# Optimization experiments

Measured on AMD Instinct MI355X. Metric: run time of the kernel, lower is better.

## Reference

```python
import jax, jax.numpy as jnp
import numpy as np

EMA_BETA = 0.9
NUM_HEADS = 16

def causal_prefix_ema(x, beta):
    # x: [b, t, d]; s_t = beta*s_{t-1} + (1-beta)*x_t, s_{-1}=0
    def step(s, xt):
        s = beta * s + (1.0 - beta) * xt
        return s, s
    s0 = jnp.zeros_like(x[:, 0, :])
    _, ys = jax.lax.scan(step, s0, jnp.swapaxes(x, 0, 1))  # [t, b, d]
    return jnp.swapaxes(ys, 0, 1)

def setup_inputs() -> dict:
    key = jax.random.key(0)
    ks = jax.random.split(key, 9)
    b, t, d = 2, 1024, 2048
    sc = lambda fan_in: 1.0 / np.sqrt(fan_in)
    return {
        "x": jax.random.normal(ks[0], (b, t, d), jnp.float32),
        "l3_memory": jax.random.normal(ks[1], (b, 1, d), jnp.float32),
        "wq": jax.random.normal(ks[2], (d, d), jnp.float32) * sc(d),
        "wk": jax.random.normal(ks[3], (d, d), jnp.float32) * sc(d),
        "wv": jax.random.normal(ks[4], (d, d), jnp.float32) * sc(d),
        "wo": jax.random.normal(ks[5], (d, d), jnp.float32) * sc(d),
        "rw1": jax.random.normal(ks[6], (d // 2, d), jnp.float32) * sc(d),
        "rb1": jnp.zeros((d // 2,), jnp.float32),
        "rw2": jax.random.normal(ks[7], (3, d // 2), jnp.float32) * sc(d // 2),
        "rb2": jnp.zeros((3,), jnp.float32),
    }

def reference(x, l3_memory, wq, wk, wv, wo, rw1, rb1, rw2, rb2):
    b, t, d = x.shape
    h = NUM_HEADS
    dh = d // h
    scale = 1.0 / np.sqrt(dh)

    q = x @ wq.T                                   # [b,t,d]
    l1 = x
    l2 = causal_prefix_ema(x, EMA_BETA)            # [b,t,d]
    l3 = jnp.broadcast_to(l3_memory, (b, t, d))    # repeat retrieval memory to length t

    # router: MLP(Q) -> softmax over 3 levels
    hdn = jax.nn.silu(q @ rw1.T + rb1)
    lam = jax.nn.softmax(hdn @ rw2.T + rb2, axis=-1)  # [b,t,3]

    fused = lam[..., 0:1] * l1 + lam[..., 1:2] * l2 + lam[..., 2:3] * l3

    def heads(y):
        return jnp.swapaxes(y.reshape(b, t, h, dh), 1, 2)  # [b,h,t,dh]

    qh = heads(q)
    kh = heads(fused @ wk.T)
    vh = heads(fused @ wv.T)

    scores = jnp.einsum("bhqd,bhkd->bhqk", qh, kh) * scale
    causal = jnp.tril(jnp.ones((t, t), bool))
    scores = jnp.where(causal, scores, jnp.finfo(scores.dtype).min)
    attn = jax.nn.softmax(scores, axis=-1)
    out = jnp.einsum("bhqk,bhkd->bhqd", attn, vh)

    out = jnp.swapaxes(out, 1, 2).reshape(b, t, d) @ wo.T
    return (out, kh, vh, lam)
```

## Files before the change

### kernel.cpp

```cpp
#include <hip/hip_runtime.h>
#include <hip/hip_bf16.h>
#include <math.h>

#define B_  2
#define T_  1024
#define D_  2048
#define H_  16
#define DH_ 128
#define M_  2048
#define DR_ 1024

typedef __attribute__((ext_vector_type(8))) short short8;
typedef __attribute__((ext_vector_type(4))) short sh4;
typedef __attribute__((ext_vector_type(4))) float f32x4;

__device__ __forceinline__ void gld16(const __hip_bfloat16* g, __hip_bfloat16* l) {
  __builtin_amdgcn_global_load_lds(
      (const __attribute__((address_space(1))) unsigned int*)g,
      (__attribute__((address_space(3))) unsigned int*)l, 16, 0, 0);
}

template<int BM, int CMODE, bool SILU>
__global__ __launch_bounds__(256)
void gemm_mfma(const __hip_bfloat16* __restrict__ A,
               const __hip_bfloat16* __restrict__ Bm,
               const float* __restrict__ bias,
               float* __restrict__ C, __hip_bfloat16* __restrict__ Cb,
               float* __restrict__ C2, __hip_bfloat16* __restrict__ Cb2,
               int M, int N, int K)
{
  constexpr int NI = BM / 32;
  constexpr int AC = BM / 64;
  __shared__ __hip_bfloat16 As[2][2][BM * 32];
  __shared__ __hip_bfloat16 Bs[2][2][128 * 32];
  const int tid  = threadIdx.x;
  const int wave = tid >> 6;
  const int lane = tid & 63;
  const int m0 = blockIdx.y * BM;
  const int n0 = blockIdx.x * 128;
  const int wm = (wave >> 1) * (BM / 2);
  const int wn = (wave & 1) * 64;

  const int srow = lane >> 2;
  const int scol = (lane & 3) * 8;
  const __hip_bfloat16* Ag = A  + (size_t)(m0 + wave * (BM / 4) + srow) * K + scol;
  const __hip_bfloat16* Bg = Bm + (size_t)(n0 + wave * 32 + srow) * K + scol;

  const int fr = lane & 15;
  const int fk = (lane >> 4) * 8;

  f32x4 acc[NI][4];
  #pragma unroll
  for (int i = 0; i < NI; ++i)
    #pragma unroll
    for (int j = 0; j < 4; ++j) acc[i][j] = (f32x4)0.f;

  auto stage = [&](int bf, int k0) {
    #pragma unroll
    for (int h = 0; h < 2; ++h) {
      #pragma unroll
      for (int c = 0; c < AC; ++c)
        gld16(Ag + k0 + h * 32 + (size_t)(c * 16) * K,
              &As[bf][h][(wave * (BM / 4) + c * 16) * 32]);
      #pragma unroll
      for (int c = 0; c < 2; ++c)
        gld16(Bg + k0 + h * 32 + (size_t)(c * 16) * K,
              &Bs[bf][h][(wave * 32 + c * 16) * 32]);
    }
  };

  stage(0, 0);
  __syncthreads();
  int cur = 0;
  for (int k0 = 0; k0 < K; k0 += 64) {
    if (k0 + 64 < K) stage(cur ^ 1, k0 + 64);
    #pragma unroll
    for (int h = 0; h < 2; ++h) {
      short8 af[NI], bfr[4];
      #pragma unroll
      for (int i = 0; i < NI; ++i)
        af[i]  = *(const short8*)&As[cur][h][(wm + i * 16 + fr) * 32 + fk];
      #pragma unroll
      for (int j = 0; j < 4; ++j)
        bfr[j] = *(const short8*)&Bs[cur][h][(wn + j * 16 + fr) * 32 + fk];
      #pragma unroll
      for (int i = 0; i < NI; ++i)
        #pragma unroll
        for (int j = 0; j < 4; ++j)
          acc[i][j] = __builtin_amdgcn_mfma_f32_16x16x32_bf16(af[i], bfr[j], acc[i][j], 0, 0, 0);
    }
    __syncthreads();
    cur ^= 1;
  }

  #pragma unroll
  for (int i = 0; i < NI; ++i) {
    #pragma unroll
    for (int j = 0; j < 4; ++j) {
      const int row0 = m0 + wm + i * 16 + (lane >> 4) * 4;
      const int col  = n0 + wn + j * 16 + (lane & 15);
      float vr[4];
      #pragma unroll
      for (int r = 0; r < 4; ++r) {
        float v = acc[i][j][r];
        if (bias) v += bias[col];
        if (SILU) v = v / (1.f + __expf(-v));
        vr[r] = v;
      }
      if (CMODE == 0) {
        #pragma unroll
        for (int r = 0; r < 4; ++r) C[(size_t)(row0 + r) * N + col] = vr[r];
      } else if (CMODE == 1) {
        #pragma unroll
        for (int r = 0; r < 4; ++r) Cb[(size_t)(row0 + r) * N + col] = __float2bfloat16(vr[r]);
      } else {
        const int bb = row0 >> 10, t0v = row0 & 1023;
        if (col < D_) {
          const int hh = col >> 7, dd = col & 127;
          #pragma unroll
          for (int r = 0; r < 4; ++r) {
            const size_t idx = (((size_t)(bb * H_ + hh)) * T_ + t0v + r) * DH_ + dd;
            C[idx] = vr[r];
            Cb[idx] = __float2bfloat16(vr[r]);
          }
        } else {
          const int c2 = col - D_;
          const int hh = c2 >> 7, dd = c2 & 127;
          #pragma unroll
          for (int r = 0; r < 4; ++r)
            C2[(((size_t)(bb * H_ + hh)) * T_ + t0v + r) * DH_ + dd] = vr[r];
          __hip_bfloat16 tmp[4];
          #pragma unroll
          for (int r = 0; r < 4; ++r) tmp[r] = __float2bfloat16(vr[r]);
          *(sh4*)(Cb2 + (((size_t)(bb * H_ + hh)) * DH_ + dd) * T_ + t0v) = *(const sh4*)tmp;
        }
      }
    }
  }
}

__global__ __launch_bounds__(256)
void cvt6(const float* __restrict__ s0, const float* __restrict__ s1,
          const float* __restrict__ s2, const float* __restrict__ s3,
          const float* __restrict__ s4, const float* __restrict__ s5,
          __hip_bfloat16* d0, __hip_bfloat16* d1, __hip_bfloat16* d2,
          __hip_bfloat16* d3, __hip_bfloat16* d4, __hip_bfloat16* d5,
          int n0, int n1, int n2, int n3, int n4, int n5)
{
  const float* s; __hip_bfloat16* d; int n;
  switch (blockIdx.y) {
    case 0: s = s0; d = d0; n = n0; break;
    case 1: s = s1; d = d1; n = n1; break;
    case 2: s = s2; d = d2; n = n2; break;
    case 3: s = s3; d = d3; n = n3; break;
    case 4: s = s4; d = d4; n = n4; break;
    default: s = s5; d = d5; n = n5; break;
  }
  const int i = (blockIdx.x * 256 + threadIdx.x) * 4;
  if (i < n) {
    float4 v = *(const float4*)(s + i);
    d[i + 0] = __float2bfloat16(v.x);
    d[i + 1] = __float2bfloat16(v.y);
    d[i + 2] = __float2bfloat16(v.z);
    d[i + 3] = __float2bfloat16(v.w);
  }
}

__global__ __launch_bounds__(256)
void ema_scan(const float* __restrict__ x, float* __restrict__ l2)
{
  const int b  = blockIdx.z;
  const int t0 = blockIdx.y * 64;
  const int d  = blockIdx.x * 256 + threadIdx.x;
  const float* xp = x  + (size_t)b * T_ * D_ + d;
  float*       lp = l2 + (size_t)b * T_ * D_ + d;
  float s = 0.f;
  #pragma unroll 4
  for (int t = t0; t < t0 + 64; ++t) {
    s = 0.9f * s + 0.1f * xp[(size_t)t * D_];
    lp[(size_t)t * D_] = s;
  }
}

__global__ __launch_bounds__(256)
void ema_carry(const float* __restrict__ l2loc, float* __restrict__ carry)
{
  const int i = blockIdx.x * 256 + threadIdx.x;
  const int b = i >> 11, d = i & 2047;
  const float A = 1.1790184577738583e-3f;
  float c = 0.f;
  carry[((size_t)b * 16 + 0) * D_ + d] = 0.f;
  for (int ch = 1; ch < 16; ++ch) {
    const float lf = l2loc[((size_t)b * T_ + ch * 64 - 1) * D_ + d];
    c = lf + A * c;
    carry[((size_t)b * 16 + ch) * D_ + d] = c;
  }
}

__global__ __launch_bounds__(256)
void router_kernel(const float* __restrict__ hdn, const float* __restrict__ rw2,
                   const float* __restrict__ rb2, float* __restrict__ lam)
{
  const int lane = threadIdx.x & 63;
  const int w    = threadIdx.x >> 6;
  const int m    = blockIdx.x * 4 + w;
  const float* hp = hdn + (size_t)m * DR_;
  float s0 = 0.f, s1 = 0.f, s2 = 0.f;
  for (int k = lane * 4; k < DR_; k += 256) {
    float4 h4 = *(const float4*)(hp + k);
    float4 w0 = *(const float4*)(rw2 + k);
    float4 w1 = *(const float4*)(rw2 + DR_ + k);
    float4 w2 = *(const float4*)(rw2 + 2 * DR_ + k);
    s0 += h4.x * w0.x + h4.y * w0.y + h4.z * w0.z + h4.w * w0.w;
    s1 += h4.x * w1.x + h4.y * w1.y + h4.z * w1.z + h4.w * w1.w;
    s2 += h4.x * w2.x + h4.y * w2.y + h4.z * w2.z + h4.w * w2.w;
  }
  #pragma unroll
  for (int off = 32; off > 0; off >>= 1) {
    s0 += __shfl_down(s0, off);
    s1 += __shfl_down(s1, off);
    s2 += __shfl_down(s2, off);
  }
  if (lane == 0) {
    s0 += rb2[0]; s1 += rb2[1]; s2 += rb2[2];
    float mx = fmaxf(s0, fmaxf(s1, s2));
    float e0 = __expf(s0 - mx), e1 = __expf(s1 - mx), e2 = __expf(s2 - mx);
    float inv = 1.f / (e0 + e1 + e2);
    lam[(size_t)m * 3 + 0] = e0 * inv;
    lam[(size_t)m * 3 + 1] = e1 * inv;
    lam[(size_t)m * 3 + 2] = e2 * inv;
  }
}

__global__ __launch_bounds__(256)
void fuse_bf16(const float* __restrict__ x, const float* __restrict__ l2,
               const float* __restrict__ l3m, const float* __restrict__ lam,
               const float* __restrict__ carry, __hip_bfloat16* __restrict__ fb)
{
  const int i4 = blockIdx.x * 256 + threadIdx.x;
  const int m  = i4 >> 9;
  const int c  = (i4 & 511) << 2;
  const int b  = m >> 10;
  const int t  = m & 1023;
  const int ch = t >> 6, off = t & 63;
  const float p = __expf((float)(off + 1) * -0.105360515657f);
  const float w0 = lam[m * 3 + 0], w1 = lam[m * 3 + 1], w2 = lam[m * 3 + 2];
  const float4 xv = *(const float4*)(x   + (size_t)m * D_ + c);
  const float4 ev = *(const float4*)(l2  + (size_t)m * D_ + c);
  const float4 gv = *(const float4*)(l3m + (size_t)b * D_ + c);
  const float4 cv = *(const float4*)(carry + ((size_t)b * 16 + ch) * D_ + c);
  __hip_bfloat16* o = fb + (size_t)m * D_ + c;
  o[0] = __float2bfloat16(w0 * xv.x + w1 * (ev.x + p * cv.x) + w2 * gv.x);
  o[1] = __float2bfloat16(w0 * xv.y + w1 * (ev.y + p * cv.y) + w2 * gv.y);
  o[2] = __float2bfloat16(w0 * xv.z + w1 * (ev.z + p * cv.z) + w2 * gv.z);
  o[3] = __float2bfloat16(w0 * xv.w + w1 * (ev.w + p * cv.w) + w2 * gv.w);
}

__global__ __launch_bounds__(256)
void flash_mfma(const __hip_bfloat16* __restrict__ qg,
                const __hip_bfloat16* __restrict__ kg,
                const __hip_bfloat16* __restrict__ vg,
                __hip_bfloat16* __restrict__ og)
{
  __shared__ __hip_bfloat16 Qs[64 * 136];
  __shared__ __hip_bfloat16 Ks[64 * 136];
  __shared__ __hip_bfloat16 Vt[128 * 72];
  __shared__ __hip_bfloat16 Ps[64 * 72];
  const int tid  = threadIdx.x;
  const int wave = tid >> 6, lane = tid & 63;
  const int qt = blockIdx.x, bh = blockIdx.y;
  const int b = bh >> 4, h = bh & 15;
  const int q0 = qt * 64;
  const int lo = lane & 15, hi = lane >> 4;

  {
    const __hip_bfloat16* qsrc = qg + (size_t)(b * T_ + q0) * D_ + h * DH_;
    #pragma unroll
    for (int i = 0; i < 4; ++i) {
      const int ci = tid + 256 * i;
      const int r = ci >> 4, j = ci & 15;
      short8 v = *(const short8*)(qsrc + (size_t)r * D_ + j * 8);
      *(short8*)&Qs[r * 136 + j * 8] = v;
    }
  }
  __syncthreads();
  short8 aq[4];
  #pragma unroll
  for (int kk = 0; kk < 4; ++kk)
    aq[kk] = *(const short8*)&Qs[(wave * 16 + lo) * 136 + kk * 32 + hi * 8];

  f32x4 oacc[8];
  #pragma unroll
  for (int i = 0; i < 8; ++i) oacc[i] = (f32x4)0.f;
  float mrow[4] = {-INFINITY, -INFINITY, -INFINITY, -INFINITY};
  float lrow[4] = {0.f, 0.f, 0.f, 0.f};

  const __hip_bfloat16* kbp = kg + (size_t)bh * T_ * DH_;
  const __hip_bfloat16* vbp = vg + (size_t)bh * DH_ * T_;
  const float scale = 0.08838834764831845f;

  for (int kt = 0; kt <= qt; ++kt) {
    const int k0 = kt * 64;
    __syncthreads();
    #pragma unroll
    for (int i = 0; i < 4; ++i) {
      const int ci = tid + 256 * i;
      const int r = ci >> 4, j = ci & 15;
      short8 v = *(const short8*)(kbp + (size_t)(k0 + r) * DH_ + j * 8);
      *(short8*)&Ks[r * 136 + j * 8] = v;
      const int dd = ci >> 3, j2 = ci & 7;
      short8 w = *(const short8*)(vbp + (size_t)dd * T_ + k0 + j2 * 8);
      *(short8*)&Vt[dd * 72 + j2 * 8] = w;
    }
    __syncthreads();

    f32x4 sc[4];
    #pragma unroll
    for (int nt = 0; nt < 4; ++nt) {
      sc[nt] = (f32x4)0.f;
      #pragma unroll
      for (int kk = 0; kk < 4; ++kk) {
        short8 bk = *(const short8*)&Ks[(nt * 16 + lo) * 136 + kk * 32 + hi * 8];
        sc[nt] = __builtin_amdgcn_mfma_f32_16x16x32_bf16(aq[kk], bk, sc[nt], 0, 0, 0);
      }
    }
    const int qrow = q0 + wave * 16 + hi * 4;
    #pragma unroll
    for (int nt = 0; nt < 4; ++nt) {
      const int key = k0 + nt * 16 + lo;
      #pragma unroll
      for (int r = 0; r < 4; ++r) {
        float v = sc[nt][r] * scale;
        sc[nt][r] = (key <= qrow + r) ? v : -1e30f;
      }
    }
    float alpha[4];
    #pragma unroll
    for (int r = 0; r < 4; ++r) {
      float mx = fmaxf(fmaxf(sc[0][r], sc[1][r]), fmaxf(sc[2][r], sc[3][r]));
      mx = fmaxf(mx, __shfl_xor(mx, 1));
      mx = fmaxf(mx, __shfl_xor(mx, 2));
      mx = fmaxf(mx, __shfl_xor(mx, 4));
      mx = fmaxf(mx, __shfl_xor(mx, 8));
      const float nm = fmaxf(mrow[r], mx);
      alpha[r] = __expf(mrow[r] - nm);
      mrow[r] = nm;
      float ls = 0.f;
      #pragma unroll
      for (int nt = 0; nt < 4; ++nt) {
        float p = __expf(sc[nt][r] - nm);
        sc[nt][r] = p;
        ls += p;
      }
      ls += __shfl_xor(ls, 1);
      ls += __shfl_xor(ls, 2);
      ls += __shfl_xor(ls, 4);
      ls += __shfl_xor(ls, 8);
      lrow[r] = lrow[r] * alpha[r] + ls;
    }
    #pragma unroll
    for (int nt = 0; nt < 4; ++nt)
      #pragma unroll
      for (int r = 0; r < 4; ++r)
        Ps[(wave * 16 + hi * 4 + r) * 72 + nt * 16 + lo] = __float2bfloat16(sc[nt][r]);
    #pragma unroll
    for (int n2 = 0; n2 < 8; ++n2)
      #pragma unroll
      for (int r = 0; r < 4; ++r) oacc[n2][r] *= alpha[r];
    short8 ap[2];
    #pragma unroll
    for (int k2 = 0; k2 < 2; ++k2)
      ap[k2] = *(const short8*)&Ps[(wave * 16 + lo) * 72 + k2 * 32 + hi * 8];
    #pragma unroll
    for (int n2 = 0; n2 < 8; ++n2) {
      #pragma unroll
      for (int k2 = 0; k2 < 2; ++k2) {
        short8 bv = *(const short8*)&Vt[(n2 * 16 + lo) * 72 + k2 * 32 + hi * 8];
        oacc[n2] = __builtin_amdgcn_mfma_f32_16x16x32_bf16(ap[k2], bv, oacc[n2], 0, 0, 0);
      }
    }
  }

  float inv[4];
  #pragma unroll
  for (int r = 0; r < 4; ++r) inv[r] = 1.f / lrow[r];
  __hip_bfloat16* od = og + (size_t)(b * T_ + q0 + wave * 16 + hi * 4) * D_ + h * DH_;
  #pragma unroll
  for (int n2 = 0; n2 < 8; ++n2)
    #pragma unroll
    for (int r = 0; r < 4; ++r)
      od[(size_t)r * D_ + n2 * 16 + lo] = __float2bfloat16(oacc[n2][r] * inv[r]);
}

extern "C" void kernel_launch(void* const* d_in, const int* in_sizes, int n_in,
                              void* d_out, int out_size, void* d_ws, size_t ws_size,
                              hipStream_t stream)
{
  const float* x   = (const float*)d_in[0];
  const float* l3m = (const float*)d_in[1];
  const float* wq  = (const float*)d_in[2];
  const float* wk  = (const float*)d_in[3];
  const float* wv  = (const float*)d_in[4];
  const float* wo  = (const float*)d_in[5];
  const float* rw1 = (const float*)d_in[6];
  const float* rb1 = (const float*)d_in[7];
  const float* rw2 = (const float*)d_in[8];
  const float* rb2 = (const float*)d_in[9];

  float* out = (float*)d_out;
  float* kh  = out + 4194304;
  float* vh  = out + 8388608;
  float* lam = out + 12582912;

  char* wsb = (char*)d_ws;
  float*          l2_f32 = (float*)(wsb);
  float*          hdn    = (float*)(wsb + (16u << 20));
  __hip_bfloat16* wkb    = (__hip_bfloat16*)(wsb + (24u << 20));
  __hip_bfloat16* wvb    = (__hip_bfloat16*)(wsb + (32u << 20));
  __hip_bfloat16* wob    = (__hip_bfloat16*)(wsb + (40u << 20));
  __hip_bfloat16* fusedb = (__hip_bfloat16*)(wsb + (48u << 20));
  __hip_bfloat16* attnb  = (__hip_bfloat16*)(wsb + (56u << 20));
  __hip_bfloat16* khb    = (__hip_bfloat16*)(wsb + (64u << 20));
  __hip_bfloat16* vtb    = (__hip_bfloat16*)(wsb + (72u << 20));
  float*          carry  = (float*)attnb;
  __hip_bfloat16* wqb  = (__hip_bfloat16*)kh;
  __hip_bfloat16* rw1b = (__hip_bfloat16*)kh + 4194304;
  __hip_bfloat16* xb   = (__hip_bfloat16*)vh;
  __hip_bfloat16* qb   = (__hip_bfloat16*)out;

  dim3 blk(256);

  cvt6<<<dim3(4096, 6), blk, 0, stream>>>(x, wq, wk, wv, wo, rw1,
                                          xb, wqb, wkb, wvb, wob, rw1b,
                                          M_ * D_, D_ * D_, D_ * D_, D_ * D_, D_ * D_, DR_ * D_);
  ema_scan<<<dim3(8, 16, 2), blk, 0, stream>>>(x, l2_f32);
  ema_carry<<<dim3(16), blk, 0, stream>>>(l2_f32, carry);
  gemm_mfma<64, 1, false><<<dim3(16, 32), blk, 0, stream>>>(xb, wqb, nullptr, nullptr, qb, nullptr, nullptr, M_, D_, D_);
  gemm_mfma<64, 0, true><<<dim3(8, 32), blk, 0, stream>>>(qb, rw1b, rb1, hdn, nullptr, nullptr, nullptr, M_, DR_, D_);
  router_kernel<<<dim3(512), blk, 0, stream>>>(hdn, rw2, rb2, lam);
  fuse_bf16<<<dim3(4096), blk, 0, stream>>>(x, l2_f32, l3m, lam, carry, fusedb);
  gemm_mfma<128, 4, false><<<dim3(32, 16), blk, 0, stream>>>(fusedb, wkb, nullptr, kh, khb, vh, vtb, M_, 2 * D_, D_);
  flash_mfma<<<dim3(16, 32), blk, 0, stream>>>(qb, khb, vtb, attnb);
  gemm_mfma<64, 0, false><<<dim3(16, 32), blk, 0, stream>>>(attnb, wob, nullptr, out, nullptr, nullptr, nullptr, M_, D_, D_);
}
```

Before: 364.1 us.

## Prefetch K/V tiles into registers and rebalance causal flash-attention block order

The flash attention kernel now loads the next K/V tile into registers while computing on the current one, so global-memory latency overlaps the MFMA work. Q is loaded straight into registers, dropping the Qs shared buffer and one barrier. The causal mask is applied only on the diagonal tile, and s_setprio is raised around the MFMA sections. Blocks are remapped onto a 1D grid so the two halves walk query tiles in opposite orders, which is meant to balance the triangular causal workload across CUs. The cost is more registers per thread for the prefetch buffers, which may lower occupancy.

```diff
diff --git a/kernel.cpp b/kernel.cpp
--- a/kernel.cpp
+++ b/kernel.cpp
@@ -262,59 +262,64 @@
                 const __hip_bfloat16* __restrict__ vg,
                 __hip_bfloat16* __restrict__ og)
 {
-  __shared__ __hip_bfloat16 Qs[64 * 136];
   __shared__ __hip_bfloat16 Ks[64 * 136];
   __shared__ __hip_bfloat16 Vt[128 * 72];
   __shared__ __hip_bfloat16 Ps[64 * 72];
   const int tid  = threadIdx.x;
   const int wave = tid >> 6, lane = tid & 63;
-  const int qt = blockIdx.x, bh = blockIdx.y;
+  const int L    = blockIdx.x;
+  const int halfg = L >> 8, idx = L & 255;
+  const int bh = (idx >> 4) | (halfg << 4);
+  const int qt = halfg ? (15 - (idx & 15)) : (idx & 15);
   const int b = bh >> 4, h = bh & 15;
   const int q0 = qt * 64;
   const int lo = lane & 15, hi = lane >> 4;
 
+  short8 aq[4];
   {
-    const __hip_bfloat16* qsrc = qg + (size_t)(b * T_ + q0) * D_ + h * DH_;
+    const __hip_bfloat16* qsrc = qg + (size_t)(b * T_ + q0 + wave * 16 + lo) * D_ + h * DH_;
+    #pragma unroll
+    for (int kk = 0; kk < 4; ++kk)
+      aq[kk] = *(const short8*)(qsrc + kk * 32 + hi * 8);
+  }
+
+  f32x4 oacc[8];
+  #pragma unroll
+  for (int i = 0; i < 8; ++i) oacc[i] = (f32x4)0.f;
+  float mrow[4] = {-INFINITY, -INFINITY, -INFINITY, -INFINITY};
+  float lrow[4] = {0.f, 0.f, 0.f, 0.f};
+
+  const __hip_bfloat16* kbp = kg + (size_t)bh * T_ * DH_;
+  const __hip_bfloat16* vbp = vg + (size_t)bh * DH_ * T_;
+  const float scale = 0.08838834764831845f;
+
+  short8 kreg[4], vreg[4];
+  auto load_tile = [&](int k0) {
     #pragma unroll
     for (int i = 0; i < 4; ++i) {
       const int ci = tid + 256 * i;
       const int r = ci >> 4, j = ci & 15;
-      short8 v = *(const short8*)(qsrc + (size_t)r * D_ + j * 8);
-      *(short8*)&Qs[r * 136 + j * 8] = v;
-    }
-  }
-  __syncthreads();
-  short8 aq[4];
-  #pragma unroll
-  for (int kk = 0; kk < 4; ++kk)
-    aq[kk] = *(const short8*)&Qs[(wave * 16 + lo) * 136 + kk * 32 + hi * 8];
-
-  f32x4 oacc[8];
-  #pragma unroll
-  for (int i = 0; i < 8; ++i) oacc[i] = (f32x4)0.f;
-  float mrow[4] = {-INFINITY, -INFINITY, -INFINITY, -INFINITY};
-  float lrow[4] = {0.f, 0.f, 0.f, 0.f};
-
-  const __hip_bfloat16* kbp = kg + (size_t)bh * T_ * DH_;
-  const __hip_bfloat16* vbp = vg + (size_t)bh * DH_ * T_;
-  const float scale = 0.08838834764831845f;
-
+      kreg[i] = *(const short8*)(kbp + (size_t)(k0 + r) * DH_ + j * 8);
+      const int dd = ci >> 3, j2 = ci & 7;
+      vreg[i] = *(const short8*)(vbp + (size_t)dd * T_ + k0 + j2 * 8);
+    }
+  };
+
+  load_tile(0);
   for (int kt = 0; kt <= qt; ++kt) {
-    const int k0 = kt * 64;
-    __syncthreads();
     #pragma unroll
     for (int i = 0; i < 4; ++i) {
       const int ci = tid + 256 * i;
       const int r = ci >> 4, j = ci & 15;
-      short8 v = *(const short8*)(kbp + (size_t)(k0 + r) * DH_ + j * 8);
-      *(short8*)&Ks[r * 136 + j * 8] = v;
+      *(short8*)&Ks[r * 136 + j * 8] = kreg[i];
       const int dd = ci >> 3, j2 = ci & 7;
-      short8 w = *(const short8*)(vbp + (size_t)dd * T_ + k0 + j2 * 8);
-      *(short8*)&Vt[dd * 72 + j2 * 8] = w;
+      *(short8*)&Vt[dd * 72 + j2 * 8] = vreg[i];
     }
     __syncthreads();
+    if (kt < qt) load_tile((kt + 1) * 64);
 
     f32x4 sc[4];
+    __builtin_amdgcn_s_setprio(1);
     #pragma unroll
     for (int nt = 0; nt < 4; ++nt) {
       sc[nt] = (f32x4)0.f;
@@ -324,14 +329,19 @@
         sc[nt] = __builtin_amdgcn_mfma_f32_16x16x32_bf16(aq[kk], bk, sc[nt], 0, 0, 0);
       }
     }
-    const int qrow = q0 + wave * 16 + hi * 4;
-    #pragma unroll
-    for (int nt = 0; nt < 4; ++nt) {
-      const int key = k0 + nt * 16 + lo;
-      #pragma unroll
-      for (int r = 0; r < 4; ++r) {
-        float v = sc[nt][r] * scale;
-        sc[nt][r] = (key <= qrow + r) ? v : -1e30f;
+    __builtin_amdgcn_s_setprio(0);
+    #pragma unroll
+    for (int nt = 0; nt < 4; ++nt)
+      #pragma unroll
+      for (int r = 0; r < 4; ++r) sc[nt][r] *= scale;
+    if (kt == qt) {
+      const int qrow = q0 + wave * 16 + hi * 4;
+      #pragma unroll
+      for (int nt = 0; nt < 4; ++nt) {
+        const int key = qt * 64 + nt * 16 + lo;
+        #pragma unroll
+        for (int r = 0; r < 4; ++r)
+          if (key > qrow + r) sc[nt][r] = -1e30f;
       }
     }
     float alpha[4];
@@ -371,6 +381,7 @@
     #pragma unroll
     for (int k2 = 0; k2 < 2; ++k2)
       ap[k2] = *(const short8*)&Ps[(wave * 16 + lo) * 72 + k2 * 32 + hi * 8];
+    __builtin_amdgcn_s_setprio(1);
     #pragma unroll
     for (int n2 = 0; n2 < 8; ++n2) {
       #pragma unroll
@@ -379,6 +390,8 @@
         oacc[n2] = __builtin_amdgcn_mfma_f32_16x16x32_bf16(ap[k2], bv, oacc[n2], 0, 0, 0);
       }
     }
+    __builtin_amdgcn_s_setprio(0);
+    __syncthreads();
   }
 
   float inv[4];
@@ -440,6 +453,6 @@
   router_kernel<<<dim3(512), blk, 0, stream>>>(hdn, rw2, rb2, lam);
   fuse_bf16<<<dim3(4096), blk, 0, stream>>>(x, l2_f32, l3m, lam, carry, fusedb);
   gemm_mfma<128, 4, false><<<dim3(32, 16), blk, 0, stream>>>(fusedb, wkb, nullptr, kh, khb, vh, vtb, M_, 2 * D_, D_);
-  flash_mfma<<<dim3(16, 32), blk, 0, stream>>>(qb, khb, vtb, attnb);
+  flash_mfma<<<dim3(512), blk, 0, stream>>>(qb, khb, vtb, attnb);
   gemm_mfma<64, 0, false><<<dim3(16, 32), blk, 0, stream>>>(attnb, wob, nullptr, out, nullptr, nullptr, nullptr, M_, D_, D_);
 }
```

Result: faster. 345.9 us (-5.0%).
